# Kernel optimization log

Hardware: AMD Instinct MI355X
Metric: run time of the kernel (lower is better)

The kernel has to match this reference:

```python
import jax, jax.numpy as jnp
import numpy as np

N_NODES = 50000
N_EDGES = 150000
NODE_F, EDGE_F = 4, 11
HID, HID_OUT = 512, 1024
VS, AS_, N_ACT = 2048, 2048, 1000


def _graph_conv(x, W, b, src, dst, n, edge_weight=None):
    # DGL GraphConv, norm='both': D_out^{-1/2} on src feats, sum-aggregate, D_in^{-1/2} on dst.
    deg_out = jnp.maximum(jnp.zeros((n,), x.dtype).at[src].add(1.0), 1.0)
    deg_in = jnp.maximum(jnp.zeros((n,), x.dtype).at[dst].add(1.0), 1.0)
    h = x * (deg_out[:, None] ** -0.5)
    mult_first = W.shape[0] > W.shape[1]
    if mult_first:
        h = h @ W
    m = h[src]  # [E, d] gather
    if edge_weight is not None:
        m = m * edge_weight  # elementwise u_mul_e
    agg = jax.ops.segment_sum(m, dst, num_segments=n)
    if not mult_first:
        agg = agg @ W
    return agg * (deg_in[:, None] ** -0.5) + b


def setup_inputs() -> dict:
    key = jax.random.key(0)
    ks = jax.random.split(key, 16)
    s = 0.05
    return {
        'node_feats': jax.random.normal(ks[0], (N_NODES, NODE_F), jnp.float32),
        'edge_feats': jax.random.normal(ks[1], (N_EDGES, EDGE_F), jnp.float32),
        'W1': jax.random.normal(ks[2], (NODE_F, EDGE_F), jnp.float32) * s,
        'b1': jnp.zeros((EDGE_F,), jnp.float32),
        'W2': jax.random.normal(ks[3], (EDGE_F, HID), jnp.float32) * s,
        'b2': jnp.zeros((HID,), jnp.float32),
        'W3': jax.random.normal(ks[4], (HID, HID_OUT), jnp.float32) * s,
        'b3': jnp.zeros((HID_OUT,), jnp.float32),
        'Wv1': jax.random.normal(ks[5], (HID_OUT, VS), jnp.float32) * s,
        'bv1': jnp.zeros((VS,), jnp.float32),
        'Wv2': jax.random.normal(ks[6], (VS, 1), jnp.float32) * s,
        'bv2': jnp.zeros((1,), jnp.float32),
        'Wa1': jax.random.normal(ks[7], (HID_OUT, AS_), jnp.float32) * s,
        'ba1': jnp.zeros((AS_,), jnp.float32),
        'Wa2': jax.random.normal(ks[8], (AS_, N_ACT), jnp.float32) * s,
        'ba2': jnp.zeros((N_ACT,), jnp.float32),
        'src': jax.random.randint(ks[9], (N_EDGES,), 0, N_NODES, jnp.int32),
        'dst': jax.random.randint(ks[10], (N_EDGES,), 0, N_NODES, jnp.int32),
    }


def reference(node_feats, edge_feats, W1, b1, W2, b2, W3, b3,
              Wv1, bv1, Wv2, bv2, Wa1, ba1, Wa2, ba2, src, dst):
    n = node_feats.shape[0]
    loop = jnp.arange(n, dtype=src.dtype)
    srcL = jnp.concatenate([src, loop])  # add_self_loop
    dstL = jnp.concatenate([dst, loop])
    # self-loop edges get zero edge features (DGL default)
    ef = jnp.concatenate([edge_feats, jnp.zeros((n, edge_feats.shape[1]), edge_feats.dtype)], axis=0)

    h = jax.nn.relu(_graph_conv(node_feats, W1, b1, srcL, dstL, n))          # [N, 11]
    h = jax.nn.relu(_graph_conv(h, W2, b2, srcL, dstL, n, edge_weight=ef))   # [N, 512]
    h = _graph_conv(h, W3, b3, srcL, dstL, n)                                # [N, 1024]

    g_emb = jnp.mean(h, axis=0, keepdims=True)  # dgl.mean_nodes, single graph -> [1, 1024]

    v = jax.nn.relu(g_emb @ Wv1 + bv1) @ Wv2 + bv2        # [1, 1]
    a = jax.nn.relu(g_emb @ Wa1 + ba1) @ Wa2 + ba2        # [1, N_ACT]
    return v + (a - a.mean())
```

## Files before the change

### kernel.cpp

```cpp
#include <hip/hip_runtime.h>

#define NN 50000
#define NE 150000
#define CAP 32

__global__ __launch_bounds__(256) void k_scat(const int* __restrict__ src,
                                              const int* __restrict__ dst,
                                              int* __restrict__ cnt_in,
                                              int* __restrict__ cnt_out,
                                              int2* __restrict__ pbuck,
                                              int* __restrict__ obuck) {
    int e = blockIdx.x * 256 + threadIdx.x;
    if (e >= NE) return;
    int s = src[e], d = dst[e];
    int si = atomicAdd(&cnt_in[d], 1) & (CAP - 1);
    pbuck[(size_t)d * CAP + si] = make_int2(e, s);
    int so = atomicAdd(&cnt_out[s], 1) & (CAP - 1);
    obuck[(size_t)s * CAP + so] = d;
}

__global__ __launch_bounds__(256) void k_node(const float* __restrict__ x,
                                              const int* __restrict__ cnt_in,
                                              const int* __restrict__ cnt_out,
                                              float* __restrict__ din_arr,
                                              float4* __restrict__ dsx4) {
    int n = blockIdx.x * 256 + threadIdx.x;
    if (n >= NN) return;
    din_arr[n] = rsqrtf((float)(cnt_in[n] + 1));
    float dout = rsqrtf((float)(cnt_out[n] + 1));
    float4 xv = ((const float4*)x)[n];
    xv.x *= dout; xv.y *= dout; xv.z *= dout; xv.w *= dout;
    dsx4[n] = xv;
}

__global__ __launch_bounds__(256) void k_conv1c(const int* __restrict__ cnt_in,
                                                const int* __restrict__ cnt_out,
                                                const int2* __restrict__ pbuck,
                                                const int* __restrict__ obuck,
                                                const float* __restrict__ din_arr,
                                                const float4* __restrict__ dsx4,
                                                const float* __restrict__ W1,
                                                const float* __restrict__ b1,
                                                float* __restrict__ h1s,
                                                float* __restrict__ c) {
    int tid = threadIdx.x;
    int n = blockIdx.x * 64 + (tid >> 2);
    int sub = tid & 3;
    if (n >= NN) return;
    int ci = cnt_in[n], co = cnt_out[n];
    float din  = rsqrtf((float)(ci + 1));
    float dout = rsqrtf((float)(co + 1));
    float a0 = 0.f, a1 = 0.f, a2 = 0.f, a3 = 0.f;
    const int2* pb = pbuck + (size_t)n * CAP;
    for (int i = sub; i < ci; i += 4) {
        int2 p = pb[i];
        float4 u = dsx4[p.y];
        a0 += u.x; a1 += u.y; a2 += u.z; a3 += u.w;
    }
    float cacc = 0.f;
    const int* ob = obuck + (size_t)n * CAP;
    for (int i = sub; i < co; i += 4) cacc += din_arr[ob[i]];
    #pragma unroll
    for (int m = 1; m < 4; m <<= 1) {
        a0 += __shfl_xor(a0, m); a1 += __shfl_xor(a1, m);
        a2 += __shfl_xor(a2, m); a3 += __shfl_xor(a3, m);
        cacc += __shfl_xor(cacc, m);
    }
    float4 sv = dsx4[n];
    a0 += sv.x; a1 += sv.y; a2 += sv.z; a3 += sv.w;
    if (sub == 0) c[n] = cacc + din;
    #pragma unroll
    for (int jj = 0; jj < 3; jj++) {
        int j = sub + 4 * jj;
        if (j < 11) {
            float y = a0 * W1[0 * 11 + j] + a1 * W1[1 * 11 + j] +
                      a2 * W1[2 * 11 + j] + a3 * W1[3 * 11 + j];
            y = fmaxf(fmaf(y, din, b1[j]), 0.f);
            h1s[(size_t)n * 11 + j] = y * dout;
        }
    }
}

__global__ __launch_bounds__(256) void k_agg2(const int* __restrict__ cnt_in,
                                              const int2* __restrict__ pbuck,
                                              const float* __restrict__ h1s,
                                              const float* __restrict__ ef,
                                              float* __restrict__ agg2) {
    int tid = threadIdx.x;
    if (tid >= 253) return;
    int q = tid / 11;
    int n = blockIdx.x * 23 + q;
    int j = tid - q * 11;
    if (n >= NN) return;
    int ci = cnt_in[n];
    const int2* pb = pbuck + (size_t)n * CAP;
    float acc = 0.f;
    for (int i = 0; i < ci; i++) {
        int2 p = pb[i];
        acc = fmaf(h1s[(size_t)p.y * 11 + j], ef[(size_t)p.x * 11 + j], acc);
    }
    agg2[(size_t)n * 11 + j] = acc;
}

#define NPB 64
__global__ __launch_bounds__(512) void k_conv2_reduce(const float* __restrict__ agg2,
                                                      const float* __restrict__ W2,
                                                      const float* __restrict__ b2,
                                                      const float* __restrict__ c,
                                                      const int* __restrict__ cnt_out,
                                                      const int* __restrict__ cnt_in,
                                                      float* __restrict__ t) {
    __shared__ float tile[NPB * 11];
    __shared__ float din_sh[NPB], w_sh[NPB];
    int n0 = blockIdx.x * NPB;
    int tid = threadIdx.x;
    for (int i = tid; i < NPB * 11; i += 512) {
        int gi = n0 * 11 + i;
        tile[i] = (gi < NN * 11) ? agg2[gi] : 0.f;
    }
    if (tid < NPB) {
        int node = n0 + tid;
        if (node < NN) {
            din_sh[tid] = rsqrtf((float)(cnt_in[node] + 1));
            w_sh[tid]   = c[node] * rsqrtf((float)(cnt_out[node] + 1)) * (1.0f / NN);
        } else { din_sh[tid] = 0.f; w_sh[tid] = 0.f; }
    }
    __syncthreads();
    float w[11];
    #pragma unroll
    for (int j = 0; j < 11; j++) w[j] = W2[j * 512 + tid];
    float bias = b2[tid];
    float acc = 0.f;
    for (int i = 0; i < NPB; i++) {
        float dot = 0.f;
        #pragma unroll
        for (int j = 0; j < 11; j++) dot = fmaf(tile[i * 11 + j], w[j], dot);
        float y = fmaxf(fmaf(dot, din_sh[i], bias), 0.f);
        acc = fmaf(w_sh[i], y, acc);
    }
    atomicAdd(&t[tid], acc);
}

__global__ __launch_bounds__(256) void k_g(const float* __restrict__ t,
                                           const float* __restrict__ W3,
                                           const float* __restrict__ b3,
                                           float* __restrict__ g) {
    int b = blockIdx.x;
    int oc = b & 3, kc = b >> 2;
    int o = oc * 256 + threadIdx.x;
    int k0 = kc * 32;
    __shared__ float ts[32];
    if (threadIdx.x < 32) ts[threadIdx.x] = t[k0 + threadIdx.x];
    __syncthreads();
    float acc = (kc == 0) ? b3[o] : 0.f;
    #pragma unroll 8
    for (int k = 0; k < 32; k++) acc = fmaf(ts[k], W3[(size_t)(k0 + k) * 1024 + o], acc);
    atomicAdd(&g[o], acc);
}

__global__ __launch_bounds__(256) void k_heads1(const float* __restrict__ g,
                                                const float* __restrict__ Wv1,
                                                const float* __restrict__ Wa1,
                                                float* __restrict__ hv_raw,
                                                float* __restrict__ ha_raw) {
    int b = blockIdx.x;
    int oc = b >> 4, kc = b & 15;
    int idx = oc * 256 + threadIdx.x;
    int k0 = kc * 64;
    __shared__ float gs[64];
    if (threadIdx.x < 64) gs[threadIdx.x] = g[k0 + threadIdx.x];
    __syncthreads();
    const float* W; float* outp; int o;
    if (idx < 2048) { W = Wv1; outp = hv_raw; o = idx; }
    else            { W = Wa1; outp = ha_raw; o = idx - 2048; }
    float acc = 0.f;
    #pragma unroll 8
    for (int k = 0; k < 64; k++) acc = fmaf(gs[k], W[(size_t)(k0 + k) * 2048 + o], acc);
    atomicAdd(&outp[o], acc);
}

__global__ __launch_bounds__(256) void k_heads2f(const float* __restrict__ hv_raw,
                                                 const float* __restrict__ bv1,
                                                 const float* __restrict__ ha_raw,
                                                 const float* __restrict__ ba1,
                                                 const float* __restrict__ Wv2,
                                                 const float* __restrict__ bv2,
                                                 const float* __restrict__ Wa2,
                                                 const float* __restrict__ ba2,
                                                 float* __restrict__ a_acc,
                                                 float* __restrict__ v,
                                                 int* __restrict__ done,
                                                 float* __restrict__ out) {
    __shared__ float sh[256];
    __shared__ int lastFlag;
    int b = blockIdx.x;
    int tid = threadIdx.x;
    if (b < 128) {
        int oc = b >> 5, kc = b & 31;
        int k0 = kc * 64;
        if (tid < 64) sh[tid] = fmaxf(ha_raw[k0 + tid] + ba1[k0 + tid], 0.f);
        __syncthreads();
        int o = oc * 256 + tid;
        if (o < 1000) {
            float acc = 0.f;
            #pragma unroll 8
            for (int k = 0; k < 64; k++)
                acc = fmaf(sh[k], Wa2[(size_t)(k0 + k) * 1000 + o], acc);
            atomicAdd(&a_acc[o], acc);
        }
    } else {
        float acc = 0.f;
        for (int k = tid; k < 2048; k += 256)
            acc = fmaf(fmaxf(hv_raw[k] + bv1[k], 0.f), Wv2[k], acc);
        sh[tid] = acc;
        __syncthreads();
        for (int s = 128; s >= 1; s >>= 1) {
            if (tid < s) sh[tid] += sh[tid + s];
            __syncthreads();
        }
        if (tid == 0) *v = sh[0] + bv2[0];
    }
    __syncthreads();
    if (tid == 0) {
        __threadfence();
        int old = atomicAdd(done, 1);
        lastFlag = (old == 128) ? 1 : 0;
    }
    __syncthreads();
    if (!lastFlag) return;
    __threadfence();
    float ai[4];
    float lsum = 0.f;
    #pragma unroll
    for (int k = 0; k < 4; k++) {
        int idx = tid + k * 256;
        float val = (idx < 1000) ? a_acc[idx] + ba2[idx] : 0.f;
        ai[k] = val;
        lsum += val;
    }
    __syncthreads();
    sh[tid] = lsum;
    __syncthreads();
    for (int s = 128; s >= 1; s >>= 1) {
        if (tid < s) sh[tid] += sh[tid + s];
        __syncthreads();
    }
    float amean = sh[0] * (1.0f / 1000.0f);
    float vv = *v;
    #pragma unroll
    for (int k = 0; k < 4; k++) {
        int idx = tid + k * 256;
        if (idx < 1000) out[idx] = vv + ai[k] - amean;
    }
}

extern "C" void kernel_launch(void* const* d_in, const int* in_sizes, int n_in,
                              void* d_out, int out_size, void* d_ws, size_t ws_size,
                              hipStream_t stream) {
    const float* x   = (const float*)d_in[0];
    const float* ef  = (const float*)d_in[1];
    const float* W1  = (const float*)d_in[2];
    const float* b1  = (const float*)d_in[3];
    const float* W2  = (const float*)d_in[4];
    const float* b2  = (const float*)d_in[5];
    const float* W3  = (const float*)d_in[6];
    const float* b3  = (const float*)d_in[7];
    const float* Wv1 = (const float*)d_in[8];
    const float* bv1 = (const float*)d_in[9];
    const float* Wv2 = (const float*)d_in[10];
    const float* bv2 = (const float*)d_in[11];
    const float* Wa1 = (const float*)d_in[12];
    const float* ba1 = (const float*)d_in[13];
    const float* Wa2 = (const float*)d_in[14];
    const float* ba2 = (const float*)d_in[15];
    const int*   src = (const int*)d_in[16];
    const int*   dst = (const int*)d_in[17];
    float* out = (float*)d_out;

    char* ws = (char*)d_ws;
    size_t off = 0;
    auto alloc = [&](size_t bytes) -> void* {
        void* p = ws + off;
        off = (off + bytes + 255) & ~(size_t)255;
        return p;
    };
    int*   cnt_in  = (int*)  alloc(NN * 4);
    int*   cnt_out = (int*)  alloc(NN * 4);
    float* t       = (float*)alloc(512 * 4);
    float* g       = (float*)alloc(1024 * 4);
    float* hv_raw  = (float*)alloc(2048 * 4);
    float* ha_raw  = (float*)alloc(2048 * 4);
    float* a_acc   = (float*)alloc(1024 * 4);
    int*   done    = (int*)  alloc(256);
    size_t zero_bytes = off;
    int2*  pbuck   = (int2*) alloc((size_t)NN * CAP * 8);
    int*   obuck   = (int*)  alloc((size_t)NN * CAP * 4);
    float* din_arr = (float*)alloc(NN * 4);
    float4* dsx4   = (float4*)alloc((size_t)NN * 16);
    float* c       = (float*)alloc(NN * 4);
    float* h1s     = (float*)alloc((size_t)NN * 11 * 4);
    float* agg2    = (float*)alloc((size_t)NN * 11 * 4);
    float* v       = (float*)alloc(256);

    hipMemsetAsync(d_ws, 0, zero_bytes, stream);

    k_scat<<<(NE + 255) / 256, 256, 0, stream>>>(src, dst, cnt_in, cnt_out, pbuck, obuck);
    k_node<<<(NN + 255) / 256, 256, 0, stream>>>(x, cnt_in, cnt_out, din_arr, dsx4);
    k_conv1c<<<(NN + 63) / 64, 256, 0, stream>>>(cnt_in, cnt_out, pbuck, obuck,
                                                 din_arr, dsx4, W1, b1, h1s, c);
    k_agg2<<<(NN + 22) / 23, 256, 0, stream>>>(cnt_in, pbuck, h1s, ef, agg2);
    k_conv2_reduce<<<(NN + NPB - 1) / NPB, 512, 0, stream>>>(agg2, W2, b2, c,
                                                             cnt_out, cnt_in, t);
    k_g<<<64, 256, 0, stream>>>(t, W3, b3, g);
    k_heads1<<<256, 256, 0, stream>>>(g, Wv1, Wa1, hv_raw, ha_raw);
    k_heads2f<<<129, 256, 0, stream>>>(hv_raw, bv1, ha_raw, ba1, Wv2, bv2, Wa2, ba2,
                                       a_acc, v, done, out);
}
```

Baseline: 185.4 us.

## Merge eight launches into two persistent kernels with software grid barriers

Collapses the graph stages (scatter, degree norm, conv1, agg2) into one kernel of 782 blocks and the conv2 reduction plus dense heads into a second kernel of 256 blocks. Stages are separated by atomic-counter grid barriers instead of kernel boundaries. The conv2 reduction now writes per-block partials that are tree-summed rather than having every block atomically add into t. This removes launch overhead and inter-kernel gaps, but it depends on all blocks being co-resident to avoid deadlock, and the barriers plus the smaller grid may cost parallelism.

```diff
diff --git a/kernel.cpp b/kernel.cpp
--- a/kernel.cpp
+++ b/kernel.cpp
@@ -3,204 +3,203 @@
 #define NN 50000
 #define NE 150000
 #define CAP 32
-
-__global__ __launch_bounds__(256) void k_scat(const int* __restrict__ src,
-                                              const int* __restrict__ dst,
-                                              int* __restrict__ cnt_in,
-                                              int* __restrict__ cnt_out,
-                                              int2* __restrict__ pbuck,
-                                              int* __restrict__ obuck) {
-    int e = blockIdx.x * 256 + threadIdx.x;
-    if (e >= NE) return;
-    int s = src[e], d = dst[e];
-    int si = atomicAdd(&cnt_in[d], 1) & (CAP - 1);
-    pbuck[(size_t)d * CAP + si] = make_int2(e, s);
-    int so = atomicAdd(&cnt_out[s], 1) & (CAP - 1);
-    obuck[(size_t)s * CAP + so] = d;
+#define GA 782
+#define GB 256
+#define NVB2 782
+#define NPB 64
+
+__device__ __forceinline__ void gbar(int* ctr, int target) {
+    __syncthreads();
+    if (threadIdx.x == 0) {
+        __threadfence();
+        __hip_atomic_fetch_add(ctr, 1, __ATOMIC_RELEASE, __HIP_MEMORY_SCOPE_AGENT);
+        while (__hip_atomic_load(ctr, __ATOMIC_RELAXED, __HIP_MEMORY_SCOPE_AGENT) < target)
+            __builtin_amdgcn_s_sleep(2);
+        __threadfence();
+    }
+    __syncthreads();
 }
 
-__global__ __launch_bounds__(256) void k_node(const float* __restrict__ x,
-                                              const int* __restrict__ cnt_in,
-                                              const int* __restrict__ cnt_out,
-                                              float* __restrict__ din_arr,
-                                              float4* __restrict__ dsx4) {
-    int n = blockIdx.x * 256 + threadIdx.x;
-    if (n >= NN) return;
-    din_arr[n] = rsqrtf((float)(cnt_in[n] + 1));
-    float dout = rsqrtf((float)(cnt_out[n] + 1));
-    float4 xv = ((const float4*)x)[n];
-    xv.x *= dout; xv.y *= dout; xv.z *= dout; xv.w *= dout;
-    dsx4[n] = xv;
+__global__ __launch_bounds__(256, 4) void k_graph(
+    const int* __restrict__ src, const int* __restrict__ dst,
+    const float* __restrict__ x, const float* __restrict__ ef,
+    const float* __restrict__ W1, const float* __restrict__ b1,
+    int* cnt_in, int* cnt_out, int2* pbuck, int* obuck,
+    float* din_arr, float* dsx4, float* c, float* h1s, float* agg2,
+    int* bar)
+{
+    int tid = threadIdx.x;
+    int gtid = blockIdx.x * 256 + tid;
+
+    if (gtid < NE) {
+        int e = gtid;
+        int s = src[e], d = dst[e];
+        int si = atomicAdd(&cnt_in[d], 1) & (CAP - 1);
+        pbuck[(size_t)d * CAP + si] = make_int2(e, s);
+        int so = atomicAdd(&cnt_out[s], 1) & (CAP - 1);
+        obuck[(size_t)s * CAP + so] = d;
+    }
+    gbar(&bar[0], GA);
+
+    if (gtid < NN) {
+        int n = gtid;
+        din_arr[n] = rsqrtf((float)(cnt_in[n] + 1));
+        float dout = rsqrtf((float)(cnt_out[n] + 1));
+        float4 xv = ((const float4*)x)[n];
+        xv.x *= dout; xv.y *= dout; xv.z *= dout; xv.w *= dout;
+        ((float4*)dsx4)[n] = xv;
+    }
+    gbar(&bar[1], GA);
+
+    {
+        int n = gtid >> 2, sub = gtid & 3;
+        if (n < NN) {
+            int ci = cnt_in[n], co = cnt_out[n];
+            float din  = rsqrtf((float)(ci + 1));
+            float dout = rsqrtf((float)(co + 1));
+            float a0 = 0.f, a1 = 0.f, a2 = 0.f, a3 = 0.f;
+            const int2* pb = pbuck + (size_t)n * CAP;
+            for (int i = sub; i < ci; i += 4) {
+                int2 p = pb[i];
+                float4 u = ((const float4*)dsx4)[p.y];
+                a0 += u.x; a1 += u.y; a2 += u.z; a3 += u.w;
+            }
+            float cacc = 0.f;
+            const int* ob = obuck + (size_t)n * CAP;
+            for (int i = sub; i < co; i += 4) cacc += din_arr[ob[i]];
+            #pragma unroll
+            for (int m = 1; m < 4; m <<= 1) {
+                a0 += __shfl_xor(a0, m); a1 += __shfl_xor(a1, m);
+                a2 += __shfl_xor(a2, m); a3 += __shfl_xor(a3, m);
+                cacc += __shfl_xor(cacc, m);
+            }
+            float4 sv = ((const float4*)dsx4)[n];
+            a0 += sv.x; a1 += sv.y; a2 += sv.z; a3 += sv.w;
+            if (sub == 0) c[n] = cacc + din;
+            #pragma unroll
+            for (int jj = 0; jj < 3; jj++) {
+                int j = sub + 4 * jj;
+                if (j < 11) {
+                    float y = a0 * W1[0 * 11 + j] + a1 * W1[1 * 11 + j] +
+                              a2 * W1[2 * 11 + j] + a3 * W1[3 * 11 + j];
+                    y = fmaxf(fmaf(y, din, b1[j]), 0.f);
+                    h1s[(size_t)n * 11 + j] = y * dout;
+                }
+            }
+        }
+    }
+    gbar(&bar[2], GA);
+
+    for (int T = gtid; T < NN * 11; T += GA * 256) {
+        int n = T / 11;
+        int j = T - n * 11;
+        int ci = cnt_in[n];
+        const int2* pb = pbuck + (size_t)n * CAP;
+        float acc = 0.f;
+        for (int i = 0; i < ci; i++) {
+            int2 p = pb[i];
+            acc = fmaf(h1s[(size_t)p.y * 11 + j], ef[(size_t)p.x * 11 + j], acc);
+        }
+        agg2[T] = acc;
+    }
 }
 
-__global__ __launch_bounds__(256) void k_conv1c(const int* __restrict__ cnt_in,
-                                                const int* __restrict__ cnt_out,
-                                                const int2* __restrict__ pbuck,
-                                                const int* __restrict__ obuck,
-                                                const float* __restrict__ din_arr,
-                                                const float4* __restrict__ dsx4,
-                                                const float* __restrict__ W1,
-                                                const float* __restrict__ b1,
-                                                float* __restrict__ h1s,
-                                                float* __restrict__ c) {
-    int tid = threadIdx.x;
-    int n = blockIdx.x * 64 + (tid >> 2);
-    int sub = tid & 3;
-    if (n >= NN) return;
-    int ci = cnt_in[n], co = cnt_out[n];
-    float din  = rsqrtf((float)(ci + 1));
-    float dout = rsqrtf((float)(co + 1));
-    float a0 = 0.f, a1 = 0.f, a2 = 0.f, a3 = 0.f;
-    const int2* pb = pbuck + (size_t)n * CAP;
-    for (int i = sub; i < ci; i += 4) {
-        int2 p = pb[i];
-        float4 u = dsx4[p.y];
-        a0 += u.x; a1 += u.y; a2 += u.z; a3 += u.w;
-    }
-    float cacc = 0.f;
-    const int* ob = obuck + (size_t)n * CAP;
-    for (int i = sub; i < co; i += 4) cacc += din_arr[ob[i]];
-    #pragma unroll
-    for (int m = 1; m < 4; m <<= 1) {
-        a0 += __shfl_xor(a0, m); a1 += __shfl_xor(a1, m);
-        a2 += __shfl_xor(a2, m); a3 += __shfl_xor(a3, m);
-        cacc += __shfl_xor(cacc, m);
-    }
-    float4 sv = dsx4[n];
-    a0 += sv.x; a1 += sv.y; a2 += sv.z; a3 += sv.w;
-    if (sub == 0) c[n] = cacc + din;
-    #pragma unroll
-    for (int jj = 0; jj < 3; jj++) {
-        int j = sub + 4 * jj;
-        if (j < 11) {
-            float y = a0 * W1[0 * 11 + j] + a1 * W1[1 * 11 + j] +
-                      a2 * W1[2 * 11 + j] + a3 * W1[3 * 11 + j];
-            y = fmaxf(fmaf(y, din, b1[j]), 0.f);
-            h1s[(size_t)n * 11 + j] = y * dout;
-        }
-    }
-}
-
-__global__ __launch_bounds__(256) void k_agg2(const int* __restrict__ cnt_in,
-                                              const int2* __restrict__ pbuck,
-                                              const float* __restrict__ h1s,
-                                              const float* __restrict__ ef,
-                                              float* __restrict__ agg2) {
-    int tid = threadIdx.x;
-    if (tid >= 253) return;
-    int q = tid / 11;
-    int n = blockIdx.x * 23 + q;
-    int j = tid - q * 11;
-    if (n >= NN) return;
-    int ci = cnt_in[n];
-    const int2* pb = pbuck + (size_t)n * CAP;
-    float acc = 0.f;
-    for (int i = 0; i < ci; i++) {
-        int2 p = pb[i];
-        acc = fmaf(h1s[(size_t)p.y * 11 + j], ef[(size_t)p.x * 11 + j], acc);
-    }
-    agg2[(size_t)n * 11 + j] = acc;
-}
-
-#define NPB 64
-__global__ __launch_bounds__(512) void k_conv2_reduce(const float* __restrict__ agg2,
-                                                      const float* __restrict__ W2,
-                                                      const float* __restrict__ b2,
-                                                      const float* __restrict__ c,
-                                                      const int* __restrict__ cnt_out,
-                                                      const int* __restrict__ cnt_in,
-                                                      float* __restrict__ t) {
+__global__ __launch_bounds__(512, 4) void k_tail(
+    const float* __restrict__ agg2, const float* __restrict__ W2, const float* __restrict__ b2,
+    const float* __restrict__ c, const int* __restrict__ cnt_in, const int* __restrict__ cnt_out,
+    const float* __restrict__ W3, const float* __restrict__ b3,
+    const float* __restrict__ Wv1, const float* __restrict__ bv1,
+    const float* __restrict__ Wv2, const float* __restrict__ bv2,
+    const float* __restrict__ Wa1, const float* __restrict__ ba1,
+    const float* __restrict__ Wa2, const float* __restrict__ ba2,
+    float* t_part, float* t, float* g, float* hv_raw, float* ha_raw,
+    float* a_acc, float* v, int* bar, float* out)
+{
     __shared__ float tile[NPB * 11];
     __shared__ float din_sh[NPB], w_sh[NPB];
-    int n0 = blockIdx.x * NPB;
-    int tid = threadIdx.x;
-    for (int i = tid; i < NPB * 11; i += 512) {
-        int gi = n0 * 11 + i;
-        tile[i] = (gi < NN * 11) ? agg2[gi] : 0.f;
-    }
-    if (tid < NPB) {
-        int node = n0 + tid;
-        if (node < NN) {
-            din_sh[tid] = rsqrtf((float)(cnt_in[node] + 1));
-            w_sh[tid]   = c[node] * rsqrtf((float)(cnt_out[node] + 1)) * (1.0f / NN);
-        } else { din_sh[tid] = 0.f; w_sh[tid] = 0.f; }
-    }
-    __syncthreads();
-    float w[11];
-    #pragma unroll
-    for (int j = 0; j < 11; j++) w[j] = W2[j * 512 + tid];
-    float bias = b2[tid];
-    float acc = 0.f;
-    for (int i = 0; i < NPB; i++) {
-        float dot = 0.f;
+    __shared__ float sh[512];
+    __shared__ int lastFlag;
+    int tid = threadIdx.x, bid = blockIdx.x;
+
+    {
+        float w[11];
         #pragma unroll
-        for (int j = 0; j < 11; j++) dot = fmaf(tile[i * 11 + j], w[j], dot);
-        float y = fmaxf(fmaf(dot, din_sh[i], bias), 0.f);
-        acc = fmaf(w_sh[i], y, acc);
-    }
-    atomicAdd(&t[tid], acc);
-}
-
-__global__ __launch_bounds__(256) void k_g(const float* __restrict__ t,
-                                           const float* __restrict__ W3,
-                                           const float* __restrict__ b3,
-                                           float* __restrict__ g) {
-    int b = blockIdx.x;
-    int oc = b & 3, kc = b >> 2;
-    int o = oc * 256 + threadIdx.x;
-    int k0 = kc * 32;
-    __shared__ float ts[32];
-    if (threadIdx.x < 32) ts[threadIdx.x] = t[k0 + threadIdx.x];
-    __syncthreads();
-    float acc = (kc == 0) ? b3[o] : 0.f;
-    #pragma unroll 8
-    for (int k = 0; k < 32; k++) acc = fmaf(ts[k], W3[(size_t)(k0 + k) * 1024 + o], acc);
-    atomicAdd(&g[o], acc);
-}
-
-__global__ __launch_bounds__(256) void k_heads1(const float* __restrict__ g,
-                                                const float* __restrict__ Wv1,
-                                                const float* __restrict__ Wa1,
-                                                float* __restrict__ hv_raw,
-                                                float* __restrict__ ha_raw) {
-    int b = blockIdx.x;
-    int oc = b >> 4, kc = b & 15;
-    int idx = oc * 256 + threadIdx.x;
-    int k0 = kc * 64;
-    __shared__ float gs[64];
-    if (threadIdx.x < 64) gs[threadIdx.x] = g[k0 + threadIdx.x];
-    __syncthreads();
-    const float* W; float* outp; int o;
-    if (idx < 2048) { W = Wv1; outp = hv_raw; o = idx; }
-    else            { W = Wa1; outp = ha_raw; o = idx - 2048; }
-    float acc = 0.f;
-    #pragma unroll 8
-    for (int k = 0; k < 64; k++) acc = fmaf(gs[k], W[(size_t)(k0 + k) * 2048 + o], acc);
-    atomicAdd(&outp[o], acc);
-}
-
-__global__ __launch_bounds__(256) void k_heads2f(const float* __restrict__ hv_raw,
-                                                 const float* __restrict__ bv1,
-                                                 const float* __restrict__ ha_raw,
-                                                 const float* __restrict__ ba1,
-                                                 const float* __restrict__ Wv2,
-                                                 const float* __restrict__ bv2,
-                                                 const float* __restrict__ Wa2,
-                                                 const float* __restrict__ ba2,
-                                                 float* __restrict__ a_acc,
-                                                 float* __restrict__ v,
-                                                 int* __restrict__ done,
-                                                 float* __restrict__ out) {
-    __shared__ float sh[256];
-    __shared__ int lastFlag;
-    int b = blockIdx.x;
-    int tid = threadIdx.x;
-    if (b < 128) {
-        int oc = b >> 5, kc = b & 31;
+        for (int j = 0; j < 11; j++) w[j] = W2[j * 512 + tid];
+        float bias = b2[tid];
+        float accT = 0.f;
+        for (int vb = bid; vb < NVB2; vb += GB) {
+            int n0 = vb * NPB;
+            __syncthreads();
+            for (int i = tid; i < NPB * 11; i += 512) {
+                int gi = n0 * 11 + i;
+                tile[i] = (gi < NN * 11) ? agg2[gi] : 0.f;
+            }
+            if (tid < NPB) {
+                int node = n0 + tid;
+                if (node < NN) {
+                    din_sh[tid] = rsqrtf((float)(cnt_in[node] + 1));
+                    w_sh[tid]   = c[node] * rsqrtf((float)(cnt_out[node] + 1)) * (1.0f / NN);
+                } else { din_sh[tid] = 0.f; w_sh[tid] = 0.f; }
+            }
+            __syncthreads();
+            for (int i = 0; i < NPB; i++) {
+                float dot = 0.f;
+                #pragma unroll
+                for (int j = 0; j < 11; j++) dot = fmaf(tile[i * 11 + j], w[j], dot);
+                float y = fmaxf(fmaf(dot, din_sh[i], bias), 0.f);
+                accT = fmaf(w_sh[i], y, accT);
+            }
+        }
+        t_part[bid * 512 + tid] = accT;
+    }
+    gbar(&bar[3], GB);
+
+    {
+        int gt = bid * 512 + tid;
+        if (gt < 16 * 512) {
+            int c16 = gt >> 9, ch = gt & 511;
+            float s = 0.f;
+            #pragma unroll
+            for (int b = 0; b < 16; b++) s += t_part[(c16 * 16 + b) * 512 + ch];
+            atomicAdd(&t[ch], s);
+        }
+    }
+    gbar(&bar[4], GB);
+
+    if (bid < 32) {
+        int oc = bid & 1, kc = bid >> 1;
+        int o = oc * 512 + tid, k0 = kc * 32;
+        float acc = (kc == 0) ? b3[o] : 0.f;
+        #pragma unroll
+        for (int k = 0; k < 32; k++)
+            acc = fmaf(t[k0 + k], W3[(size_t)(k0 + k) * 1024 + o], acc);
+        atomicAdd(&g[o], acc);
+    }
+    gbar(&bar[5], GB);
+
+    if (bid < 128) {
+        int oc = bid >> 4, kc = bid & 15;
+        int idx = oc * 512 + tid;
+        int k0 = kc * 64;
+        if (tid < 64) sh[tid] = g[k0 + tid];
+        __syncthreads();
+        const float* W; float* outp; int o;
+        if (idx < 2048) { W = Wv1; outp = hv_raw; o = idx; }
+        else            { W = Wa1; outp = ha_raw; o = idx - 2048; }
+        float acc = 0.f;
+        #pragma unroll 8
+        for (int k = 0; k < 64; k++)
+            acc = fmaf(sh[k], W[(size_t)(k0 + k) * 2048 + o], acc);
+        atomicAdd(&outp[o], acc);
+    }
+    gbar(&bar[6], GB);
+
+    if (bid < 64) {
+        int oc = bid >> 5, kc = bid & 31;
         int k0 = kc * 64;
         if (tid < 64) sh[tid] = fmaxf(ha_raw[k0 + tid] + ba1[k0 + tid], 0.f);
         __syncthreads();
-        int o = oc * 256 + tid;
+        int o = oc * 512 + tid;
         if (o < 1000) {
             float acc = 0.f;
             #pragma unroll 8
@@ -208,50 +207,42 @@
                 acc = fmaf(sh[k], Wa2[(size_t)(k0 + k) * 1000 + o], acc);
             atomicAdd(&a_acc[o], acc);
         }
-    } else {
+    } else if (bid == 64) {
         float acc = 0.f;
-        for (int k = tid; k < 2048; k += 256)
+        for (int k = tid; k < 2048; k += 512)
             acc = fmaf(fmaxf(hv_raw[k] + bv1[k], 0.f), Wv2[k], acc);
         sh[tid] = acc;
         __syncthreads();
-        for (int s = 128; s >= 1; s >>= 1) {
-            if (tid < s) sh[tid] += sh[tid + s];
+        for (int s2 = 256; s2 >= 1; s2 >>= 1) {
+            if (tid < s2) sh[tid] += sh[tid + s2];
             __syncthreads();
         }
         if (tid == 0) *v = sh[0] + bv2[0];
     }
+
     __syncthreads();
     if (tid == 0) {
         __threadfence();
-        int old = atomicAdd(done, 1);
-        lastFlag = (old == 128) ? 1 : 0;
+        int old = __hip_atomic_fetch_add(&bar[7], 1, __ATOMIC_ACQ_REL, __HIP_MEMORY_SCOPE_AGENT);
+        lastFlag = (old == GB - 1) ? 1 : 0;
     }
     __syncthreads();
     if (!lastFlag) return;
     __threadfence();
-    float ai[4];
-    float lsum = 0.f;
-    #pragma unroll
-    for (int k = 0; k < 4; k++) {
-        int idx = tid + k * 256;
-        float val = (idx < 1000) ? a_acc[idx] + ba2[idx] : 0.f;
-        ai[k] = val;
-        lsum += val;
-    }
-    __syncthreads();
-    sh[tid] = lsum;
-    __syncthreads();
-    for (int s = 128; s >= 1; s >>= 1) {
-        if (tid < s) sh[tid] += sh[tid + s];
+    int i0 = tid, i1 = tid + 512;
+    float ai0 = (i0 < 1000) ? a_acc[i0] + ba2[i0] : 0.f;
+    float ai1 = (i1 < 1000) ? a_acc[i1] + ba2[i1] : 0.f;
+    __syncthreads();
+    sh[tid] = ai0 + ai1;
+    __syncthreads();
+    for (int s2 = 256; s2 >= 1; s2 >>= 1) {
+        if (tid < s2) sh[tid] += sh[tid + s2];
         __syncthreads();
     }
     float amean = sh[0] * (1.0f / 1000.0f);
     float vv = *v;
-    #pragma unroll
-    for (int k = 0; k < 4; k++) {
-        int idx = tid + k * 256;
-        if (idx < 1000) out[idx] = vv + ai[k] - amean;
-    }
+    if (i0 < 1000) out[i0] = vv + ai0 - amean;
+    if (i1 < 1000) out[i1] = vv + ai1 - amean;
 }
 
 extern "C" void kernel_launch(void* const* d_in, const int* in_sizes, int n_in,
@@ -291,28 +282,24 @@
     float* hv_raw  = (float*)alloc(2048 * 4);
     float* ha_raw  = (float*)alloc(2048 * 4);
     float* a_acc   = (float*)alloc(1024 * 4);
-    int*   done    = (int*)  alloc(256);
+    int*   bar     = (int*)  alloc(8 * 4);
     size_t zero_bytes = off;
     int2*  pbuck   = (int2*) alloc((size_t)NN * CAP * 8);
     int*   obuck   = (int*)  alloc((size_t)NN * CAP * 4);
     float* din_arr = (float*)alloc(NN * 4);
-    float4* dsx4   = (float4*)alloc((size_t)NN * 16);
+    float* dsx4    = (float*)alloc((size_t)NN * 16);
     float* c       = (float*)alloc(NN * 4);
     float* h1s     = (float*)alloc((size_t)NN * 11 * 4);
     float* agg2    = (float*)alloc((size_t)NN * 11 * 4);
+    float* t_part  = (float*)alloc((size_t)GB * 512 * 4);
     float* v       = (float*)alloc(256);
 
     hipMemsetAsync(d_ws, 0, zero_bytes, stream);
 
-    k_scat<<<(NE + 255) / 256, 256, 0, stream>>>(src, dst, cnt_in, cnt_out, pbuck, obuck);
-    k_node<<<(NN + 255) / 256, 256, 0, stream>>>(x, cnt_in, cnt_out, din_arr, dsx4);
-    k_conv1c<<<(NN + 63) / 64, 256, 0, stream>>>(cnt_in, cnt_out, pbuck, obuck,
-                                                 din_arr, dsx4, W1, b1, h1s, c);
-    k_agg2<<<(NN + 22) / 23, 256, 0, stream>>>(cnt_in, pbuck, h1s, ef, agg2);
-    k_conv2_reduce<<<(NN + NPB - 1) / NPB, 512, 0, stream>>>(agg2, W2, b2, c,
-                                                             cnt_out, cnt_in, t);
-    k_g<<<64, 256, 0, stream>>>(t, W3, b3, g);
-    k_heads1<<<256, 256, 0, stream>>>(g, Wv1, Wa1, hv_raw, ha_raw);
-    k_heads2f<<<129, 256, 0, stream>>>(hv_raw, bv1, ha_raw, ba1, Wv2, bv2, Wa2, ba2,
-                                       a_acc, v, done, out);
+    k_graph<<<GA, 256, 0, stream>>>(src, dst, x, ef, W1, b1,
+                                    cnt_in, cnt_out, pbuck, obuck,
+                                    din_arr, dsx4, c, h1s, agg2, bar);
+    k_tail<<<GB, 512, 0, stream>>>(agg2, W2, b2, c, cnt_in, cnt_out,
+                                   W3, b3, Wv1, bv1, Wv2, bv2, Wa1, ba1, Wa2, ba2,
+                                   t_part, t, g, hv_raw, ha_raw, a_acc, v, bar, out);
 }
```

Result: slower. 529.0 us (+185.3%).

## Fuse node-normalization into conv1 and replace float atomics with partial-sum buffers

Applied to the files above, without the earlier changes.

Removes the k_node kernel by recomputing the degree normalizations on the fly inside k_conv1c from the counts and raw x. The conv2 reduction now runs as a persistent grid of 128 blocks that each write a partial row, and k_g, k_heads1 and k_heads2f reduce those partial buffers instead of using float atomicAdd into zeroed accumulators. The intent is one fewer launch, less intermediate traffic, less atomic contention and a smaller memset, at the cost of redundant rsqrt work and count loads in the gather loops.

```diff
diff --git a/kernel.cpp b/kernel.cpp
--- a/kernel.cpp
+++ b/kernel.cpp
@@ -3,6 +3,9 @@
 #define NN 50000
 #define NE 150000
 #define CAP 32
+#define NPB 64
+#define NVB2 782
+#define GC2 128
 
 __global__ __launch_bounds__(256) void k_scat(const int* __restrict__ src,
                                               const int* __restrict__ dst,
@@ -19,33 +22,17 @@
     obuck[(size_t)s * CAP + so] = d;
 }
 
-__global__ __launch_bounds__(256) void k_node(const float* __restrict__ x,
-                                              const int* __restrict__ cnt_in,
-                                              const int* __restrict__ cnt_out,
-                                              float* __restrict__ din_arr,
-                                              float4* __restrict__ dsx4) {
-    int n = blockIdx.x * 256 + threadIdx.x;
-    if (n >= NN) return;
-    din_arr[n] = rsqrtf((float)(cnt_in[n] + 1));
-    float dout = rsqrtf((float)(cnt_out[n] + 1));
-    float4 xv = ((const float4*)x)[n];
-    xv.x *= dout; xv.y *= dout; xv.z *= dout; xv.w *= dout;
-    dsx4[n] = xv;
-}
-
 __global__ __launch_bounds__(256) void k_conv1c(const int* __restrict__ cnt_in,
                                                 const int* __restrict__ cnt_out,
                                                 const int2* __restrict__ pbuck,
                                                 const int* __restrict__ obuck,
-                                                const float* __restrict__ din_arr,
-                                                const float4* __restrict__ dsx4,
+                                                const float* __restrict__ x,
                                                 const float* __restrict__ W1,
                                                 const float* __restrict__ b1,
                                                 float* __restrict__ h1s,
                                                 float* __restrict__ c) {
-    int tid = threadIdx.x;
-    int n = blockIdx.x * 64 + (tid >> 2);
-    int sub = tid & 3;
+    int gtid = blockIdx.x * 256 + threadIdx.x;
+    int n = gtid >> 2, sub = gtid & 3;
     if (n >= NN) return;
     int ci = cnt_in[n], co = cnt_out[n];
     float din  = rsqrtf((float)(ci + 1));
@@ -54,20 +41,23 @@
     const int2* pb = pbuck + (size_t)n * CAP;
     for (int i = sub; i < ci; i += 4) {
         int2 p = pb[i];
-        float4 u = dsx4[p.y];
-        a0 += u.x; a1 += u.y; a2 += u.z; a3 += u.w;
+        float os = rsqrtf((float)(cnt_out[p.y] + 1));
+        float4 u = ((const float4*)x)[p.y];
+        a0 = fmaf(u.x, os, a0); a1 = fmaf(u.y, os, a1);
+        a2 = fmaf(u.z, os, a2); a3 = fmaf(u.w, os, a3);
     }
     float cacc = 0.f;
     const int* ob = obuck + (size_t)n * CAP;
-    for (int i = sub; i < co; i += 4) cacc += din_arr[ob[i]];
+    for (int i = sub; i < co; i += 4) cacc += rsqrtf((float)(cnt_in[ob[i]] + 1));
     #pragma unroll
     for (int m = 1; m < 4; m <<= 1) {
         a0 += __shfl_xor(a0, m); a1 += __shfl_xor(a1, m);
         a2 += __shfl_xor(a2, m); a3 += __shfl_xor(a3, m);
         cacc += __shfl_xor(cacc, m);
     }
-    float4 sv = dsx4[n];
-    a0 += sv.x; a1 += sv.y; a2 += sv.z; a3 += sv.w;
+    float4 sv = ((const float4*)x)[n];
+    a0 = fmaf(sv.x, dout, a0); a1 = fmaf(sv.y, dout, a1);
+    a2 = fmaf(sv.z, dout, a2); a3 = fmaf(sv.w, dout, a3);
     if (sub == 0) c[n] = cacc + din;
     #pragma unroll
     for (int jj = 0; jj < 3; jj++) {
@@ -102,86 +92,113 @@
     agg2[(size_t)n * 11 + j] = acc;
 }
 
-#define NPB 64
 __global__ __launch_bounds__(512) void k_conv2_reduce(const float* __restrict__ agg2,
                                                       const float* __restrict__ W2,
                                                       const float* __restrict__ b2,
                                                       const float* __restrict__ c,
+                                                      const int* __restrict__ cnt_in,
                                                       const int* __restrict__ cnt_out,
-                                                      const int* __restrict__ cnt_in,
-                                                      float* __restrict__ t) {
+                                                      float* __restrict__ t_part) {
     __shared__ float tile[NPB * 11];
     __shared__ float din_sh[NPB], w_sh[NPB];
-    int n0 = blockIdx.x * NPB;
-    int tid = threadIdx.x;
-    for (int i = tid; i < NPB * 11; i += 512) {
-        int gi = n0 * 11 + i;
-        tile[i] = (gi < NN * 11) ? agg2[gi] : 0.f;
-    }
-    if (tid < NPB) {
-        int node = n0 + tid;
-        if (node < NN) {
-            din_sh[tid] = rsqrtf((float)(cnt_in[node] + 1));
-            w_sh[tid]   = c[node] * rsqrtf((float)(cnt_out[node] + 1)) * (1.0f / NN);
-        } else { din_sh[tid] = 0.f; w_sh[tid] = 0.f; }
-    }
-    __syncthreads();
+    int tid = threadIdx.x, bid = blockIdx.x;
     float w[11];
     #pragma unroll
     for (int j = 0; j < 11; j++) w[j] = W2[j * 512 + tid];
     float bias = b2[tid];
-    float acc = 0.f;
-    for (int i = 0; i < NPB; i++) {
-        float dot = 0.f;
-        #pragma unroll
-        for (int j = 0; j < 11; j++) dot = fmaf(tile[i * 11 + j], w[j], dot);
-        float y = fmaxf(fmaf(dot, din_sh[i], bias), 0.f);
-        acc = fmaf(w_sh[i], y, acc);
-    }
-    atomicAdd(&t[tid], acc);
-}
-
-__global__ __launch_bounds__(256) void k_g(const float* __restrict__ t,
+    float accT = 0.f;
+    for (int vb = bid; vb < NVB2; vb += GC2) {
+        int n0 = vb * NPB;
+        __syncthreads();
+        for (int i = tid; i < NPB * 11; i += 512) {
+            int gi = n0 * 11 + i;
+            tile[i] = (gi < NN * 11) ? agg2[gi] : 0.f;
+        }
+        if (tid < NPB) {
+            int node = n0 + tid;
+            if (node < NN) {
+                din_sh[tid] = rsqrtf((float)(cnt_in[node] + 1));
+                w_sh[tid]   = c[node] * rsqrtf((float)(cnt_out[node] + 1)) * (1.0f / NN);
+            } else { din_sh[tid] = 0.f; w_sh[tid] = 0.f; }
+        }
+        __syncthreads();
+        for (int i = 0; i < NPB; i++) {
+            float dot = 0.f;
+            #pragma unroll
+            for (int j = 0; j < 11; j++) dot = fmaf(tile[i * 11 + j], w[j], dot);
+            float y = fmaxf(fmaf(dot, din_sh[i], bias), 0.f);
+            accT = fmaf(w_sh[i], y, accT);
+        }
+    }
+    t_part[bid * 512 + tid] = accT;
+}
+
+__global__ __launch_bounds__(256) void k_g(const float* __restrict__ t_part,
                                            const float* __restrict__ W3,
                                            const float* __restrict__ b3,
-                                           float* __restrict__ g) {
+                                           float* __restrict__ g_part) {
+    __shared__ float red[256];
+    __shared__ float ts[32];
     int b = blockIdx.x;
     int oc = b & 3, kc = b >> 2;
-    int o = oc * 256 + threadIdx.x;
+    int tid = threadIdx.x;
     int k0 = kc * 32;
-    __shared__ float ts[32];
-    if (threadIdx.x < 32) ts[threadIdx.x] = t[k0 + threadIdx.x];
-    __syncthreads();
+    {
+        int ch = tid & 31, grp = tid >> 5;
+        float s = 0.f;
+        #pragma unroll
+        for (int p = 0; p < 16; p++)
+            s += t_part[(grp * 16 + p) * 512 + k0 + ch];
+        red[tid] = s;
+        __syncthreads();
+        if (tid < 32) {
+            float s2 = 0.f;
+            #pragma unroll
+            for (int gp = 0; gp < 8; gp++) s2 += red[gp * 32 + tid];
+            ts[tid] = s2;
+        }
+        __syncthreads();
+    }
+    int o = oc * 256 + tid;
     float acc = (kc == 0) ? b3[o] : 0.f;
     #pragma unroll 8
     for (int k = 0; k < 32; k++) acc = fmaf(ts[k], W3[(size_t)(k0 + k) * 1024 + o], acc);
-    atomicAdd(&g[o], acc);
-}
-
-__global__ __launch_bounds__(256) void k_heads1(const float* __restrict__ g,
+    g_part[kc * 1024 + o] = acc;
+}
+
+__global__ __launch_bounds__(256) void k_heads1(const float* __restrict__ g_part,
                                                 const float* __restrict__ Wv1,
                                                 const float* __restrict__ Wa1,
-                                                float* __restrict__ hv_raw,
-                                                float* __restrict__ ha_raw) {
+                                                float* __restrict__ h_part) {
+    __shared__ float red[256];
+    __shared__ float gs[64];
     int b = blockIdx.x;
     int oc = b >> 4, kc = b & 15;
-    int idx = oc * 256 + threadIdx.x;
+    int tid = threadIdx.x;
     int k0 = kc * 64;
-    __shared__ float gs[64];
-    if (threadIdx.x < 64) gs[threadIdx.x] = g[k0 + threadIdx.x];
-    __syncthreads();
-    const float* W; float* outp; int o;
-    if (idx < 2048) { W = Wv1; outp = hv_raw; o = idx; }
-    else            { W = Wa1; outp = ha_raw; o = idx - 2048; }
+    {
+        int ch = tid & 63, grp = tid >> 6;
+        float s = 0.f;
+        #pragma unroll
+        for (int p = 0; p < 4; p++)
+            s += g_part[(grp * 4 + p) * 1024 + k0 + ch];
+        red[tid] = s;
+        __syncthreads();
+        if (tid < 64) gs[tid] = red[tid] + red[64 + tid] + red[128 + tid] + red[192 + tid];
+        __syncthreads();
+    }
+    int idx = oc * 256 + tid;
+    const float* W; int o;
+    if (idx < 2048) { W = Wv1; o = idx; }
+    else            { W = Wa1; o = idx - 2048; }
     float acc = 0.f;
     #pragma unroll 8
     for (int k = 0; k < 64; k++) acc = fmaf(gs[k], W[(size_t)(k0 + k) * 2048 + o], acc);
-    atomicAdd(&outp[o], acc);
-}
-
-__global__ __launch_bounds__(256) void k_heads2f(const float* __restrict__ hv_raw,
+    h_part[kc * 4096 + idx] = acc;
+}
+
+__global__ __launch_bounds__(256) void k_heads2f(const float* __restrict__ h_part,
                                                  const float* __restrict__ bv1,
-                                                 const float* __restrict__ ha_raw,
                                                  const float* __restrict__ ba1,
                                                  const float* __restrict__ Wv2,
                                                  const float* __restrict__ bv2,
@@ -198,7 +215,12 @@
     if (b < 128) {
         int oc = b >> 5, kc = b & 31;
         int k0 = kc * 64;
-        if (tid < 64) sh[tid] = fmaxf(ha_raw[k0 + tid] + ba1[k0 + tid], 0.f);
+        if (tid < 64) {
+            float ha = 0.f;
+            #pragma unroll
+            for (int p = 0; p < 16; p++) ha += h_part[p * 4096 + 2048 + k0 + tid];
+            sh[tid] = fmaxf(ha + ba1[k0 + tid], 0.f);
+        }
         __syncthreads();
         int o = oc * 256 + tid;
         if (o < 1000) {
@@ -210,12 +232,16 @@
         }
     } else {
         float acc = 0.f;
-        for (int k = tid; k < 2048; k += 256)
-            acc = fmaf(fmaxf(hv_raw[k] + bv1[k], 0.f), Wv2[k], acc);
+        for (int k = tid; k < 2048; k += 256) {
+            float hv = 0.f;
+            #pragma unroll
+            for (int p = 0; p < 16; p++) hv += h_part[p * 4096 + k];
+            acc = fmaf(fmaxf(hv + bv1[k], 0.f), Wv2[k], acc);
+        }
         sh[tid] = acc;
         __syncthreads();
-        for (int s = 128; s >= 1; s >>= 1) {
-            if (tid < s) sh[tid] += sh[tid + s];
+        for (int s2 = 128; s2 >= 1; s2 >>= 1) {
+            if (tid < s2) sh[tid] += sh[tid + s2];
             __syncthreads();
         }
         if (tid == 0) *v = sh[0] + bv2[0];
@@ -241,8 +267,8 @@
     __syncthreads();
     sh[tid] = lsum;
     __syncthreads();
-    for (int s = 128; s >= 1; s >>= 1) {
-        if (tid < s) sh[tid] += sh[tid + s];
+    for (int s2 = 128; s2 >= 1; s2 >>= 1) {
+        if (tid < s2) sh[tid] += sh[tid + s2];
         __syncthreads();
     }
     float amean = sh[0] * (1.0f / 1000.0f);
@@ -286,33 +312,28 @@
     };
     int*   cnt_in  = (int*)  alloc(NN * 4);
     int*   cnt_out = (int*)  alloc(NN * 4);
-    float* t       = (float*)alloc(512 * 4);
-    float* g       = (float*)alloc(1024 * 4);
-    float* hv_raw  = (float*)alloc(2048 * 4);
-    float* ha_raw  = (float*)alloc(2048 * 4);
     float* a_acc   = (float*)alloc(1024 * 4);
     int*   done    = (int*)  alloc(256);
     size_t zero_bytes = off;
     int2*  pbuck   = (int2*) alloc((size_t)NN * CAP * 8);
     int*   obuck   = (int*)  alloc((size_t)NN * CAP * 4);
-    float* din_arr = (float*)alloc(NN * 4);
-    float4* dsx4   = (float4*)alloc((size_t)NN * 16);
     float* c       = (float*)alloc(NN * 4);
     float* h1s     = (float*)alloc((size_t)NN * 11 * 4);
     float* agg2    = (float*)alloc((size_t)NN * 11 * 4);
+    float* t_part  = (float*)alloc((size_t)GC2 * 512 * 4);
+    float* g_part  = (float*)alloc((size_t)16 * 1024 * 4);
+    float* h_part  = (float*)alloc((size_t)16 * 4096 * 4);
     float* v       = (float*)alloc(256);
 
     hipMemsetAsync(d_ws, 0, zero_bytes, stream);
 
     k_scat<<<(NE + 255) / 256, 256, 0, stream>>>(src, dst, cnt_in, cnt_out, pbuck, obuck);
-    k_node<<<(NN + 255) / 256, 256, 0, stream>>>(x, cnt_in, cnt_out, din_arr, dsx4);
     k_conv1c<<<(NN + 63) / 64, 256, 0, stream>>>(cnt_in, cnt_out, pbuck, obuck,
-                                                 din_arr, dsx4, W1, b1, h1s, c);
+                                                 x, W1, b1, h1s, c);
     k_agg2<<<(NN + 22) / 23, 256, 0, stream>>>(cnt_in, pbuck, h1s, ef, agg2);
-    k_conv2_reduce<<<(NN + NPB - 1) / NPB, 512, 0, stream>>>(agg2, W2, b2, c,
-                                                             cnt_out, cnt_in, t);
-    k_g<<<64, 256, 0, stream>>>(t, W3, b3, g);
-    k_heads1<<<256, 256, 0, stream>>>(g, Wv1, Wa1, hv_raw, ha_raw);
-    k_heads2f<<<129, 256, 0, stream>>>(hv_raw, bv1, ha_raw, ba1, Wv2, bv2, Wa2, ba2,
+    k_conv2_reduce<<<GC2, 512, 0, stream>>>(agg2, W2, b2, c, cnt_in, cnt_out, t_part);
+    k_g<<<64, 256, 0, stream>>>(t_part, W3, b3, g_part);
+    k_heads1<<<256, 256, 0, stream>>>(g_part, Wv1, Wa1, h_part);
+    k_heads2f<<<129, 256, 0, stream>>>(h_part, bv1, ba1, Wv2, bv2, Wa2, ba2,
                                        a_acc, v, done, out);
 }
```

New measurement: 200.5 us. 1.08x slower.

## Fuse edge aggregation into conv2 reduce and fold W3 matvec into heads

Applied to the files above, without the earlier changes.

Merges the layer-2 edge gather/aggregation into the conv2 reduction kernel so the aggregated tile is built directly in shared memory, removing the agg2 global round trip and one launch. It also folds the t·W3 matvec into the first head kernel: each block recomputes the 64 g entries it needs, which removes the k_g launch and the g atomics. The cost is redundant W3 reads across the 16 output-chunk blocks and fewer threads doing the gather (704 items over 512 threads, so a second pass for some).

```diff
diff --git a/kernel.cpp b/kernel.cpp
--- a/kernel.cpp
+++ b/kernel.cpp
@@ -3,6 +3,7 @@
 #define NN 50000
 #define NE 150000
 #define CAP 32
+#define NPB 64
 
 __global__ __launch_bounds__(256) void k_scat(const int* __restrict__ src,
                                               const int* __restrict__ dst,
@@ -81,42 +82,32 @@
     }
 }
 
-__global__ __launch_bounds__(256) void k_agg2(const int* __restrict__ cnt_in,
-                                              const int2* __restrict__ pbuck,
-                                              const float* __restrict__ h1s,
-                                              const float* __restrict__ ef,
-                                              float* __restrict__ agg2) {
-    int tid = threadIdx.x;
-    if (tid >= 253) return;
-    int q = tid / 11;
-    int n = blockIdx.x * 23 + q;
-    int j = tid - q * 11;
-    if (n >= NN) return;
-    int ci = cnt_in[n];
-    const int2* pb = pbuck + (size_t)n * CAP;
-    float acc = 0.f;
-    for (int i = 0; i < ci; i++) {
-        int2 p = pb[i];
-        acc = fmaf(h1s[(size_t)p.y * 11 + j], ef[(size_t)p.x * 11 + j], acc);
-    }
-    agg2[(size_t)n * 11 + j] = acc;
-}
-
-#define NPB 64
-__global__ __launch_bounds__(512) void k_conv2_reduce(const float* __restrict__ agg2,
-                                                      const float* __restrict__ W2,
-                                                      const float* __restrict__ b2,
-                                                      const float* __restrict__ c,
-                                                      const int* __restrict__ cnt_out,
-                                                      const int* __restrict__ cnt_in,
-                                                      float* __restrict__ t) {
+__global__ __launch_bounds__(512) void k_agg2conv2(const int* __restrict__ cnt_in,
+                                                   const int* __restrict__ cnt_out,
+                                                   const int2* __restrict__ pbuck,
+                                                   const float* __restrict__ h1s,
+                                                   const float* __restrict__ ef,
+                                                   const float* __restrict__ W2,
+                                                   const float* __restrict__ b2,
+                                                   const float* __restrict__ c,
+                                                   float* __restrict__ t) {
     __shared__ float tile[NPB * 11];
     __shared__ float din_sh[NPB], w_sh[NPB];
+    int tid = threadIdx.x;
     int n0 = blockIdx.x * NPB;
-    int tid = threadIdx.x;
-    for (int i = tid; i < NPB * 11; i += 512) {
-        int gi = n0 * 11 + i;
-        tile[i] = (gi < NN * 11) ? agg2[gi] : 0.f;
+    for (int idx = tid; idx < NPB * 11; idx += 512) {
+        int q = idx / 11, j = idx - q * 11;
+        int n = n0 + q;
+        float acc = 0.f;
+        if (n < NN) {
+            int ci = cnt_in[n];
+            const int2* pb = pbuck + (size_t)n * CAP;
+            for (int i = 0; i < ci; i++) {
+                int2 p = pb[i];
+                acc = fmaf(h1s[(size_t)p.y * 11 + j], ef[(size_t)p.x * 11 + j], acc);
+            }
+        }
+        tile[idx] = acc;
     }
     if (tid < NPB) {
         int node = n0 + tid;
@@ -141,41 +132,45 @@
     atomicAdd(&t[tid], acc);
 }
 
-__global__ __launch_bounds__(256) void k_g(const float* __restrict__ t,
-                                           const float* __restrict__ W3,
-                                           const float* __restrict__ b3,
-                                           float* __restrict__ g) {
-    int b = blockIdx.x;
-    int oc = b & 3, kc = b >> 2;
-    int o = oc * 256 + threadIdx.x;
-    int k0 = kc * 32;
-    __shared__ float ts[32];
-    if (threadIdx.x < 32) ts[threadIdx.x] = t[k0 + threadIdx.x];
-    __syncthreads();
-    float acc = (kc == 0) ? b3[o] : 0.f;
-    #pragma unroll 8
-    for (int k = 0; k < 32; k++) acc = fmaf(ts[k], W3[(size_t)(k0 + k) * 1024 + o], acc);
-    atomicAdd(&g[o], acc);
-}
-
-__global__ __launch_bounds__(256) void k_heads1(const float* __restrict__ g,
-                                                const float* __restrict__ Wv1,
-                                                const float* __restrict__ Wa1,
-                                                float* __restrict__ hv_raw,
-                                                float* __restrict__ ha_raw) {
+__global__ __launch_bounds__(256) void k_heads1g(const float* __restrict__ t,
+                                                 const float* __restrict__ W3,
+                                                 const float* __restrict__ b3,
+                                                 const float* __restrict__ Wv1,
+                                                 const float* __restrict__ Wa1,
+                                                 float* __restrict__ hv_raw,
+                                                 float* __restrict__ ha_raw) {
+    __shared__ float ts[512];
+    __shared__ float gpart[256];
+    __shared__ float gs[64];
     int b = blockIdx.x;
     int oc = b >> 4, kc = b & 15;
-    int idx = oc * 256 + threadIdx.x;
+    int tid = threadIdx.x;
     int k0 = kc * 64;
-    __shared__ float gs[64];
-    if (threadIdx.x < 64) gs[threadIdx.x] = g[k0 + threadIdx.x];
-    __syncthreads();
+    ts[tid] = t[tid];
+    ts[tid + 256] = t[tid + 256];
+    __syncthreads();
+    {
+        int i = tid & 63, kp = tid >> 6;
+        float p = 0.f;
+        int kb = kp * 128;
+        #pragma unroll 8
+        for (int k = 0; k < 128; k++)
+            p = fmaf(ts[kb + k], W3[(size_t)(kb + k) * 1024 + k0 + i], p);
+        gpart[tid] = p;
+        __syncthreads();
+        if (tid < 64)
+            gs[tid] = b3[k0 + tid] + gpart[tid] + gpart[64 + tid] +
+                      gpart[128 + tid] + gpart[192 + tid];
+        __syncthreads();
+    }
+    int idx = oc * 256 + tid;
     const float* W; float* outp; int o;
     if (idx < 2048) { W = Wv1; outp = hv_raw; o = idx; }
     else            { W = Wa1; outp = ha_raw; o = idx - 2048; }
     float acc = 0.f;
     #pragma unroll 8
-    for (int k = 0; k < 64; k++) acc = fmaf(gs[k], W[(size_t)(k0 + k) * 2048 + o], acc);
+    for (int k = 0; k < 64; k++)
+        acc = fmaf(gs[k], W[(size_t)(k0 + k) * 2048 + o], acc);
     atomicAdd(&outp[o], acc);
 }
 
@@ -214,8 +209,8 @@
             acc = fmaf(fmaxf(hv_raw[k] + bv1[k], 0.f), Wv2[k], acc);
         sh[tid] = acc;
         __syncthreads();
-        for (int s = 128; s >= 1; s >>= 1) {
-            if (tid < s) sh[tid] += sh[tid + s];
+        for (int s2 = 128; s2 >= 1; s2 >>= 1) {
+            if (tid < s2) sh[tid] += sh[tid + s2];
             __syncthreads();
         }
         if (tid == 0) *v = sh[0] + bv2[0];
@@ -241,8 +236,8 @@
     __syncthreads();
     sh[tid] = lsum;
     __syncthreads();
-    for (int s = 128; s >= 1; s >>= 1) {
-        if (tid < s) sh[tid] += sh[tid + s];
+    for (int s2 = 128; s2 >= 1; s2 >>= 1) {
+        if (tid < s2) sh[tid] += sh[tid + s2];
         __syncthreads();
     }
     float amean = sh[0] * (1.0f / 1000.0f);
@@ -287,7 +282,6 @@
     int*   cnt_in  = (int*)  alloc(NN * 4);
     int*   cnt_out = (int*)  alloc(NN * 4);
     float* t       = (float*)alloc(512 * 4);
-    float* g       = (float*)alloc(1024 * 4);
     float* hv_raw  = (float*)alloc(2048 * 4);
     float* ha_raw  = (float*)alloc(2048 * 4);
     float* a_acc   = (float*)alloc(1024 * 4);
@@ -299,7 +293,6 @@
     float4* dsx4   = (float4*)alloc((size_t)NN * 16);
     float* c       = (float*)alloc(NN * 4);
     float* h1s     = (float*)alloc((size_t)NN * 11 * 4);
-    float* agg2    = (float*)alloc((size_t)NN * 11 * 4);
     float* v       = (float*)alloc(256);
 
     hipMemsetAsync(d_ws, 0, zero_bytes, stream);
@@ -308,11 +301,9 @@
     k_node<<<(NN + 255) / 256, 256, 0, stream>>>(x, cnt_in, cnt_out, din_arr, dsx4);
     k_conv1c<<<(NN + 63) / 64, 256, 0, stream>>>(cnt_in, cnt_out, pbuck, obuck,
                                                  din_arr, dsx4, W1, b1, h1s, c);
-    k_agg2<<<(NN + 22) / 23, 256, 0, stream>>>(cnt_in, pbuck, h1s, ef, agg2);
-    k_conv2_reduce<<<(NN + NPB - 1) / NPB, 512, 0, stream>>>(agg2, W2, b2, c,
-                                                             cnt_out, cnt_in, t);
-    k_g<<<64, 256, 0, stream>>>(t, W3, b3, g);
-    k_heads1<<<256, 256, 0, stream>>>(g, Wv1, Wa1, hv_raw, ha_raw);
+    k_agg2conv2<<<(NN + NPB - 1) / NPB, 512, 0, stream>>>(cnt_in, cnt_out, pbuck,
+                                                          h1s, ef, W2, b2, c, t);
+    k_heads1g<<<256, 256, 0, stream>>>(t, W3, b3, Wv1, Wa1, hv_raw, ha_raw);
     k_heads2f<<<129, 256, 0, stream>>>(hv_raw, bv1, ha_raw, ba1, Wv2, bv2, Wa2, ba2,
                                        a_acc, v, done, out);
 }
```

Result: no change. 188.8 us (+1.8%).
